# Kernel tuning notes

Measured on AMD Instinct MI355X. Metric: run time of the kernel, lower is better.

Reference implementation:

```python
import jax, jax.numpy as jnp
import numpy as np

MOMENTUM = 0.999
TEMP = 0.07
NUM_HARD_NEGS = 16
NUM_CLASSES = 20000


def _normalize(x, axis=-1, eps=1e-12):
    n = jnp.linalg.norm(x, axis=axis, keepdims=True)
    return x / jnp.maximum(n, eps)


def setup_inputs() -> dict:
    key = jax.random.key(0)
    k1, k2, k3, k4, k5 = jax.random.split(key, 5)
    B, K, Dp, De, C = 512, 8, 256, 512, NUM_CLASSES
    return {
        "part_features": jax.random.normal(k1, (B, K, Dp), dtype=jnp.float32),
        "embeddings": jax.random.normal(k2, (B, De), dtype=jnp.float32),
        "sat_emb": jax.random.normal(k3, (B, De), dtype=jnp.float32),
        "part_bank": jax.random.normal(k4, (C, K, Dp), dtype=jnp.float32) * 0.01,
        "embed_bank": jax.random.normal(k5, (C, De), dtype=jnp.float32) * 0.01,
        "labels": jnp.arange(B, dtype=jnp.int64),
    }


def reference(part_features, embeddings, sat_emb, part_bank, embed_bank, labels):
    m = MOMENTUM
    B = embeddings.shape[0]
    C = embed_bank.shape[0]

    # --- EMA scatter update (bank assumed initialized for all classes) ---
    # labels are distinct, so vectorized scatter == sequential python loop.
    new_part_bank = part_bank.at[labels].set(
        m * part_bank[labels] + (1.0 - m) * part_features)
    new_embed_bank = embed_bank.at[labels].set(
        m * embed_bank[labels] + (1.0 - m) * embeddings)

    # Banks are torch buffers updated under no_grad -> stop_gradient.
    eb = jax.lax.stop_gradient(new_embed_bank)

    # --- PrototypeNCE ---
    q = _normalize(embeddings)                      # [B, De]
    protos = _normalize(eb)                         # [C, De]
    sim = (q @ protos.T) / TEMP                     # [B, C]
    pos_sim = jnp.take_along_axis(sim, labels[:, None], axis=1)  # [B, 1]
    class_ids = jnp.arange(C)
    pos_mask = labels[:, None] == class_ids[None, :]
    neg_sim = jnp.where(pos_mask, -1e9, sim)
    hard_negs, _ = jax.lax.top_k(neg_sim, NUM_HARD_NEGS)          # [B, k]
    logits = jnp.concatenate([pos_sim, hard_negs], axis=1)       # [B, 1+k]
    nce_loss = jnp.mean(jax.nn.logsumexp(logits, axis=1) - logits[:, 0])

    # --- Cross-view prototype alignment ---
    p = _normalize(eb[labels])                      # [B, De]
    d = _normalize(embeddings)
    s = _normalize(sat_emb)
    align_loss = 0.5 * (jnp.mean(1.0 - jnp.sum(d * p, axis=-1))
                        + jnp.mean(1.0 - jnp.sum(s * p, axis=-1)))

    return new_part_bank, new_embed_bank, nce_loss, align_loss
```

## Files before the change

kernel.cpp:

```cpp
#include <hip/hip_runtime.h>
#include <math.h>

#define MOM 0.999f
#define ONE_M_MOM 0.001f
#define INV_TEMP (1.0f / 0.07f)
#define C_CLASSES 20000
#define B_SZ 512
#define DE 512
#define PART_ROW 2048
#define PART_BANK_N (C_CLASSES * PART_ROW)
#define EMB_BANK_N (C_CLASSES * DE)
#define NEG_INF (-3.0e38f)
#define NTILE 157
#define NT2 (NTILE * 2)
#define NGEMM (4 * NTILE)
#define NPART 2500

typedef __attribute__((ext_vector_type(8))) short short8;
typedef __attribute__((ext_vector_type(4))) float f32x4;

__device__ inline unsigned short f2bf_rne(float f) {
    unsigned u = __builtin_bit_cast(unsigned, f);
    return (unsigned short)((u + 0x7FFFu + ((u >> 16) & 1u)) >> 16);
}

__device__ inline float bf2f(unsigned short u) {
    return __builtin_bit_cast(float, (unsigned)u << 16);
}

__device__ inline void gload16(const void* g, void* l) {
    __builtin_amdgcn_global_load_lds(
        (const __attribute__((address_space(1))) unsigned int*)g,
        (__attribute__((address_space(3))) unsigned int*)l, 16, 0, 0);
}

__global__ void embed_qnorm(const float* __restrict__ ebank, const float* __restrict__ emb,
                            const int* __restrict__ labels, float* __restrict__ out_eb,
                            unsigned short* __restrict__ Bb, float* __restrict__ inv_norm,
                            float* __restrict__ q_hat, unsigned short* __restrict__ Ab,
                            int* __restrict__ counter) {
    int w = threadIdx.x >> 6, l = threadIdx.x & 63;
    int blk = blockIdx.x;
    if (blk == 0 && threadIdx.x == 0) *counter = 0;
    if (blk < 5000) {
        int c = blk * 4 + w;
        int m = -1;
#pragma unroll
        for (int k = 0; k < 8; ++k)
            if (labels[l + k * 64] == c) m = l + k * 64;
#pragma unroll
        for (int off = 32; off; off >>= 1) m = max(m, __shfl_xor(m, off));

        const float4* row = (const float4*)(ebank + ((long)c << 9));
        float4 v0 = row[2 * l], v1 = row[2 * l + 1];
        if (m >= 0) {
            const float4* nr = (const float4*)(emb + ((long)m << 9));
            float4 n0 = nr[2 * l], n1 = nr[2 * l + 1];
            v0.x = MOM * v0.x + ONE_M_MOM * n0.x;
            v0.y = MOM * v0.y + ONE_M_MOM * n0.y;
            v0.z = MOM * v0.z + ONE_M_MOM * n0.z;
            v0.w = MOM * v0.w + ONE_M_MOM * n0.w;
            v1.x = MOM * v1.x + ONE_M_MOM * n1.x;
            v1.y = MOM * v1.y + ONE_M_MOM * n1.y;
            v1.z = MOM * v1.z + ONE_M_MOM * n1.z;
            v1.w = MOM * v1.w + ONE_M_MOM * n1.w;
        }
        float4* orow = (float4*)(out_eb + ((long)c << 9));
        orow[2 * l] = v0; orow[2 * l + 1] = v1;
        float ss = v0.x * v0.x + v0.y * v0.y + v0.z * v0.z + v0.w * v0.w
                 + v1.x * v1.x + v1.y * v1.y + v1.z * v1.z + v1.w * v1.w;
#pragma unroll
        for (int off = 32; off; off >>= 1) ss += __shfl_xor(ss, off);
        if (l == 0) inv_norm[c] = 1.0f / fmaxf(sqrtf(ss), 1e-12f);
        short8 o;
        o[0] = (short)f2bf_rne(v0.x); o[1] = (short)f2bf_rne(v0.y);
        o[2] = (short)f2bf_rne(v0.z); o[3] = (short)f2bf_rne(v0.w);
        o[4] = (short)f2bf_rne(v1.x); o[5] = (short)f2bf_rne(v1.y);
        o[6] = (short)f2bf_rne(v1.z); o[7] = (short)f2bf_rne(v1.w);
        *(short8*)(Bb + ((long)c << 9) + l * 8) = o;
    } else {
        int b = (blk - 5000) * 4 + w;
        const float4* row = (const float4*)(emb + ((long)b << 9));
        float4 v0 = row[2 * l], v1 = row[2 * l + 1];
        float ss = v0.x * v0.x + v0.y * v0.y + v0.z * v0.z + v0.w * v0.w
                 + v1.x * v1.x + v1.y * v1.y + v1.z * v1.z + v1.w * v1.w;
#pragma unroll
        for (int off = 32; off; off >>= 1) ss += __shfl_xor(ss, off);
        float inv = 1.0f / fmaxf(sqrtf(ss), 1e-12f);
        v0.x *= inv; v0.y *= inv; v0.z *= inv; v0.w *= inv;
        v1.x *= inv; v1.y *= inv; v1.z *= inv; v1.w *= inv;
        float4* outq = (float4*)(q_hat + ((long)b << 9));
        outq[2 * l] = v0; outq[2 * l + 1] = v1;
        short8 o;
        o[0] = (short)f2bf_rne(v0.x); o[1] = (short)f2bf_rne(v0.y);
        o[2] = (short)f2bf_rne(v0.z); o[3] = (short)f2bf_rne(v0.w);
        o[4] = (short)f2bf_rne(v1.x); o[5] = (short)f2bf_rne(v1.y);
        o[6] = (short)f2bf_rne(v1.z); o[7] = (short)f2bf_rne(v1.w);
        *(short8*)(Ab + ((long)b << 9) + l * 8) = o;
    }
}

__global__ void __launch_bounds__(256)
part_gemm(const unsigned short* __restrict__ A, const unsigned short* __restrict__ B,
          const float* __restrict__ inv_norm, const int* __restrict__ labels,
          float* __restrict__ partials,
          const float4* __restrict__ pb, const float4* __restrict__ pf,
          float4* __restrict__ out_pb) {
    __shared__ unsigned short smem[128 * 130];

    if (blockIdx.x >= NGEMM) {
        int c0 = (blockIdx.x - NGEMM) * 8;
        int t = threadIdx.x;
        int* mbs = (int*)smem;
        if (t < 8) mbs[t] = -1;
        __syncthreads();
        int la = labels[t], lb = labels[t + 256];
#pragma unroll
        for (int r = 0; r < 8; ++r) {
            if (la == c0 + r) mbs[r] = t;
            if (lb == c0 + r) mbs[r] = t + 256;
        }
        __syncthreads();
        const float4* src = pb + (long)c0 * (PART_ROW / 4);
        float4* dst = out_pb + (long)c0 * (PART_ROW / 4);
        float4 v[16];
#pragma unroll
        for (int i = 0; i < 16; ++i) v[i] = src[t + i * 256];
#pragma unroll
        for (int i = 0; i < 16; ++i) {
            int mb = mbs[i >> 1];
            if (mb >= 0) {
                float4 n = pf[(long)mb * (PART_ROW / 4) + (t + (i & 1) * 256)];
                v[i].x = MOM * v[i].x + ONE_M_MOM * n.x;
                v[i].y = MOM * v[i].y + ONE_M_MOM * n.y;
                v[i].z = MOM * v[i].z + ONE_M_MOM * n.z;
                v[i].w = MOM * v[i].w + ONE_M_MOM * n.w;
            }
            dst[t + i * 256] = v[i];
        }
        return;
    }

    unsigned short* Asm = smem;
    unsigned short* Bsm = smem + 8192;

    const int t = threadIdx.x;
    const int w = t >> 6, l = t & 63;
    const int wr = w >> 1, wc = w & 1;

    int id = blockIdx.x;
    int xcd = id & 7, idx = id >> 3;
    int wg = (xcd < 4) ? xcd * 79 + idx : 316 + (xcd - 4) * 78 + idx;
    const int bm = wg & 3, bn = wg >> 2;

    f32x4 acc[4][4] = {};

    const int srow = t >> 3;
    const long swz = ((t & 7) ^ (srow & 7)) << 3;
    const unsigned short* Ag = A + ((long)(bm * 128 + srow) << 9) + swz;
    const unsigned short* Bg[4];
#pragma unroll
    for (int i = 0; i < 4; ++i) {
        int br = bn * 128 + i * 32 + srow;
        if (br > C_CLASSES - 1) br = C_CLASSES - 1;
        Bg[i] = B + ((long)br << 9) + swz;
    }
    char* Adst = (char*)Asm + (w << 10);
    char* Bdst = (char*)Bsm + (w << 10);

    const int fr = l & 15;
    const int s4 = l >> 4;
    const int swr0 = ((s4) ^ (fr & 7)) << 4;
    const int swr1 = ((4 + s4) ^ (fr & 7)) << 4;

    for (int kt = 0; kt < 8; ++kt) {
        const int ko = kt << 6;
#pragma unroll
        for (int i = 0; i < 4; ++i) {
            gload16(Ag + ko + ((long)i << 14), Adst + (i << 12));
            gload16(Bg[i] + ko, Bdst + (i << 12));
        }
        __syncthreads();
        short8 af[2][4], bf[2][4];
        const char* Abase = (const char*)Asm;
        const char* Bbase = (const char*)Bsm;
#pragma unroll
        for (int m = 0; m < 4; ++m) {
            int ra = (wr * 64 + m * 16 + fr) << 7;
            int rb = (wc * 64 + m * 16 + fr) << 7;
            af[0][m] = *(const short8*)(Abase + ra + swr0);
            af[1][m] = *(const short8*)(Abase + ra + swr1);
            bf[0][m] = *(const short8*)(Bbase + rb + swr0);
            bf[1][m] = *(const short8*)(Bbase + rb + swr1);
        }
#pragma unroll
        for (int kk = 0; kk < 2; ++kk)
#pragma unroll
            for (int m = 0; m < 4; ++m)
#pragma unroll
                for (int n = 0; n < 4; ++n)
                    acc[m][n] = __builtin_amdgcn_mfma_f32_16x16x32_bf16(
                        af[kk][m], bf[kk][n], acc[m][n], 0, 0, 0);
        __syncthreads();
    }

    unsigned short* stile = smem;
    const int r4 = s4 << 2;
#pragma unroll
    for (int n = 0; n < 4; ++n) {
        int ct = wc * 64 + fr + n * 16;
        int cg = bn * 128 + ct;
        bool ok = cg < C_CLASSES;
        float sc = ok ? inv_norm[cg] * INV_TEMP : 0.0f;
#pragma unroll
        for (int m = 0; m < 4; ++m) {
            int rt = wr * 64 + r4 + m * 16;
#pragma unroll
            for (int j = 0; j < 4; ++j) {
                float v = ok ? acc[m][n][j] * sc : NEG_INF;
                stile[(rt + j) * 130 + ct] = f2bf_rne(v);
            }
        }
    }
    __syncthreads();

    const int r = t >> 1, half = t & 1;
    const int gr = bm * 128 + r;
    const int lab = labels[gr];
    const int lab_l = lab - (bn << 7) - (half << 6);
    const unsigned short* bp = stile + r * 130 + half * 64;
    float tl[16];
#pragma unroll
    for (int j = 0; j < 16; ++j) tl[j] = NEG_INF;
    for (int c = 0; c < 64; ++c) {
        if (c == lab_l) continue;
        float v = bf2f(bp[c]);
        if (v > tl[15]) {
            tl[15] = v;
#pragma unroll
            for (int j = 15; j > 0; --j) {
                float a = tl[j - 1], bb = tl[j];
                if (bb > a) { tl[j - 1] = bb; tl[j] = a; }
            }
        }
    }
    float* op = partials + ((long)gr * NT2 + (bn << 1) + half) * 16;
#pragma unroll
    for (int j = 0; j < 16; ++j) op[j] = tl[j];
}

__global__ void __launch_bounds__(64)
merge_fin(const float* __restrict__ partials, const float* __restrict__ q_hat,
          const float* __restrict__ out_eb, const float* __restrict__ sat,
          const float* __restrict__ inv_norm, const int* __restrict__ labels,
          float* __restrict__ lnce, float* __restrict__ lalign,
          int* __restrict__ counter, float* __restrict__ out_losses) {
    int b = blockIdx.x;
    int l = threadIdx.x;
    const float4* pr4 = (const float4*)(partials + (long)b * (NT2 * 16));

    float tl[16];
#pragma unroll
    for (int j = 0; j < 16; ++j) tl[j] = NEG_INF;
    for (int i = l; i < NT2 * 4; i += 64) {
        float4 v4 = pr4[i];
        float vv[4] = {v4.x, v4.y, v4.z, v4.w};
#pragma unroll
        for (int q = 0; q < 4; ++q) {
            float v = vv[q];
            if (v > tl[15]) {
                tl[15] = v;
#pragma unroll
                for (int j = 15; j > 0; --j) {
                    float a = tl[j - 1], bb = tl[j];
                    if (bb > a) { tl[j - 1] = bb; tl[j] = a; }
                }
            }
        }
    }

    float M = 0.f, S = 0.f;
#pragma unroll 1
    for (int j = 0; j < 16; ++j) {
        float v = tl[0];
        float mx = v;
#pragma unroll
        for (int off = 32; off; off >>= 1) mx = fmaxf(mx, __shfl_xor(mx, off));
        unsigned long long ball = __ballot(v == mx);
        int win = (int)(__ffsll((unsigned long long)ball)) - 1;
        if (l == win) {
#pragma unroll
            for (int q = 0; q < 15; ++q) tl[q] = tl[q + 1];
            tl[15] = NEG_INF;
        }
        if (j == 0) { M = mx; S = 1.0f; }
        else S += expf(mx - M);
    }

    int lab = labels[b];
    const float4* qr = (const float4*)(q_hat + ((long)b << 9));
    const float4* er = (const float4*)(out_eb + ((long)lab << 9));
    const float4* sr = (const float4*)(sat + ((long)b << 9));
    float a1 = 0.f, a2 = 0.f, a3 = 0.f;
#pragma unroll
    for (int rr = 0; rr < 2; ++rr) {
        int j = 2 * l + rr;
        float4 d4 = qr[j], s4 = sr[j], e4 = er[j];
        a1 += d4.x * e4.x + d4.y * e4.y + d4.z * e4.z + d4.w * e4.w;
        a2 += s4.x * e4.x + s4.y * e4.y + s4.z * e4.z + s4.w * e4.w;
        a3 += s4.x * s4.x + s4.y * s4.y + s4.z * s4.z + s4.w * s4.w;
    }
#pragma unroll
    for (int off = 32; off; off >>= 1) {
        a1 += __shfl_xor(a1, off);
        a2 += __shfl_xor(a2, off);
        a3 += __shfl_xor(a3, off);
    }
    int done = 0;
    if (l == 0) {
        float invl = inv_norm[lab];
        float pos = a1 * invl * INV_TEMP;
        float mx2 = fmaxf(M, pos);
        float ssum = expf(M - mx2) * S + expf(pos - mx2);
        lnce[b] = logf(ssum) + mx2 - pos;
        float pd = a1 * invl;
        float ps = a2 * invl / fmaxf(sqrtf(a3), 1e-12f);
        lalign[b] = 1.0f - 0.5f * (pd + ps);
        __threadfence();
        done = (atomicAdd(counter, 1) == B_SZ - 1) ? 1 : 0;
    }
    done = __shfl(done, 0);
    if (done) {
        __threadfence();
        volatile const float* vn = lnce;
        volatile const float* va = lalign;
        float s1 = 0.f, s2 = 0.f;
#pragma unroll
        for (int k = 0; k < B_SZ / 64; ++k) {
            s1 += vn[l + k * 64];
            s2 += va[l + k * 64];
        }
#pragma unroll
        for (int off = 32; off; off >>= 1) {
            s1 += __shfl_xor(s1, off);
            s2 += __shfl_xor(s2, off);
        }
        if (l == 0) {
            out_losses[0] = s1 / (float)B_SZ;
            out_losses[1] = s2 / (float)B_SZ;
            *counter = 0;
        }
    }
}

extern "C" void kernel_launch(void* const* d_in, const int* in_sizes, int n_in,
                              void* d_out, int out_size, void* d_ws, size_t ws_size,
                              hipStream_t stream) {
    const float* pf = (const float*)d_in[0];
    const float* emb = (const float*)d_in[1];
    const float* sat = (const float*)d_in[2];
    const float* pb = (const float*)d_in[3];
    const float* ebank = (const float*)d_in[4];
    const int* labels = (const int*)d_in[5];

    float* out = (float*)d_out;
    float* out_pb = out;
    float* out_eb = out + PART_BANK_N;
    float* out_losses = out + PART_BANK_N + EMB_BANK_N;

    float* ws = (float*)d_ws;
    float* q_hat = ws;
    float* inv_norm = q_hat + (long)B_SZ * DE;
    int* counter = (int*)(inv_norm + C_CLASSES);
    float* lnce = (float*)(counter + 16);
    float* lalign = lnce + B_SZ;
    float* partials = lalign + B_SZ;
    unsigned short* Ab = (unsigned short*)(partials + (long)B_SZ * NT2 * 16);
    unsigned short* Bb = Ab + (long)B_SZ * DE;

    embed_qnorm<<<5000 + 128, 256, 0, stream>>>(ebank, emb, labels, out_eb, Bb, inv_norm,
                                                q_hat, Ab, counter);
    part_gemm<<<NGEMM + NPART, 256, 0, stream>>>(Ab, Bb, inv_norm, labels, partials,
                                                 (const float4*)pb, (const float4*)pf,
                                                 (float4*)out_pb);
    merge_fin<<<B_SZ, 64, 0, stream>>>(partials, q_hat, out_eb, sat, inv_norm,
                                       labels, lnce, lalign, counter, out_losses);
}
```

Before: 146.3 us.

## Persist part-bank copy blocks, merge half-tile top-k in GEMM, drop q_hat buffer

Result: slower. 157.1 us (+7.4%).

```diff
diff --git a/kernel.cpp b/kernel.cpp
--- a/kernel.cpp
+++ b/kernel.cpp
@@ -12,9 +12,9 @@
 #define EMB_BANK_N (C_CLASSES * DE)
 #define NEG_INF (-3.0e38f)
 #define NTILE 157
-#define NT2 (NTILE * 2)
 #define NGEMM (4 * NTILE)
-#define NPART 2500
+#define NCHUNK 2500
+#define NPARTB 512
 
 typedef __attribute__((ext_vector_type(8))) short short8;
 typedef __attribute__((ext_vector_type(4))) float f32x4;
@@ -37,8 +37,7 @@
 __global__ void embed_qnorm(const float* __restrict__ ebank, const float* __restrict__ emb,
                             const int* __restrict__ labels, float* __restrict__ out_eb,
                             unsigned short* __restrict__ Bb, float* __restrict__ inv_norm,
-                            float* __restrict__ q_hat, unsigned short* __restrict__ Ab,
-                            int* __restrict__ counter) {
+                            unsigned short* __restrict__ Ab, int* __restrict__ counter) {
     int w = threadIdx.x >> 6, l = threadIdx.x & 63;
     int blk = blockIdx.x;
     if (blk == 0 && threadIdx.x == 0) *counter = 0;
@@ -89,8 +88,6 @@
         float inv = 1.0f / fmaxf(sqrtf(ss), 1e-12f);
         v0.x *= inv; v0.y *= inv; v0.z *= inv; v0.w *= inv;
         v1.x *= inv; v1.y *= inv; v1.z *= inv; v1.w *= inv;
-        float4* outq = (float4*)(q_hat + ((long)b << 9));
-        outq[2 * l] = v0; outq[2 * l + 1] = v1;
         short8 o;
         o[0] = (short)f2bf_rne(v0.x); o[1] = (short)f2bf_rne(v0.y);
         o[2] = (short)f2bf_rne(v0.z); o[3] = (short)f2bf_rne(v0.w);
@@ -109,34 +106,37 @@
     __shared__ unsigned short smem[128 * 130];
 
     if (blockIdx.x >= NGEMM) {
-        int c0 = (blockIdx.x - NGEMM) * 8;
         int t = threadIdx.x;
         int* mbs = (int*)smem;
-        if (t < 8) mbs[t] = -1;
-        __syncthreads();
         int la = labels[t], lb = labels[t + 256];
-#pragma unroll
-        for (int r = 0; r < 8; ++r) {
-            if (la == c0 + r) mbs[r] = t;
-            if (lb == c0 + r) mbs[r] = t + 256;
-        }
-        __syncthreads();
-        const float4* src = pb + (long)c0 * (PART_ROW / 4);
-        float4* dst = out_pb + (long)c0 * (PART_ROW / 4);
-        float4 v[16];
-#pragma unroll
-        for (int i = 0; i < 16; ++i) v[i] = src[t + i * 256];
-#pragma unroll
-        for (int i = 0; i < 16; ++i) {
-            int mb = mbs[i >> 1];
-            if (mb >= 0) {
-                float4 n = pf[(long)mb * (PART_ROW / 4) + (t + (i & 1) * 256)];
-                v[i].x = MOM * v[i].x + ONE_M_MOM * n.x;
-                v[i].y = MOM * v[i].y + ONE_M_MOM * n.y;
-                v[i].z = MOM * v[i].z + ONE_M_MOM * n.z;
-                v[i].w = MOM * v[i].w + ONE_M_MOM * n.w;
+        for (int chunk = blockIdx.x - NGEMM; chunk < NCHUNK; chunk += NPARTB) {
+            int c0 = chunk * 8;
+            __syncthreads();
+            if (t < 8) mbs[t] = -1;
+            __syncthreads();
+#pragma unroll
+            for (int r = 0; r < 8; ++r) {
+                if (la == c0 + r) mbs[r] = t;
+                if (lb == c0 + r) mbs[r] = t + 256;
             }
-            dst[t + i * 256] = v[i];
+            __syncthreads();
+            const float4* src = pb + (long)c0 * (PART_ROW / 4);
+            float4* dst = out_pb + (long)c0 * (PART_ROW / 4);
+            float4 v[16];
+#pragma unroll
+            for (int i = 0; i < 16; ++i) v[i] = src[t + i * 256];
+#pragma unroll
+            for (int i = 0; i < 16; ++i) {
+                int mb = mbs[i >> 1];
+                if (mb >= 0) {
+                    float4 n = pf[(long)mb * (PART_ROW / 4) + (t + (i & 1) * 256)];
+                    v[i].x = MOM * v[i].x + ONE_M_MOM * n.x;
+                    v[i].y = MOM * v[i].y + ONE_M_MOM * n.y;
+                    v[i].z = MOM * v[i].z + ONE_M_MOM * n.z;
+                    v[i].w = MOM * v[i].w + ONE_M_MOM * n.w;
+                }
+                dst[t + i * 256] = v[i];
+            }
         }
         return;
     }
@@ -193,6 +193,7 @@
             bf[0][m] = *(const short8*)(Bbase + rb + swr0);
             bf[1][m] = *(const short8*)(Bbase + rb + swr1);
         }
+        __builtin_amdgcn_s_setprio(1);
 #pragma unroll
         for (int kk = 0; kk < 2; ++kk)
 #pragma unroll
@@ -201,6 +202,7 @@
                 for (int n = 0; n < 4; ++n)
                     acc[m][n] = __builtin_amdgcn_mfma_f32_16x16x32_bf16(
                         af[kk][m], bf[kk][n], acc[m][n], 0, 0, 0);
+        __builtin_amdgcn_s_setprio(0);
         __syncthreads();
     }
 
@@ -244,25 +246,38 @@
             }
         }
     }
-    float* op = partials + ((long)gr * NT2 + (bn << 1) + half) * 16;
-#pragma unroll
-    for (int j = 0; j < 16; ++j) op[j] = tl[j];
+    float ol[16];
+#pragma unroll
+    for (int j = 0; j < 16; ++j) ol[j] = __shfl_xor(tl[j], 1);
+    if (half == 0) {
+        float4 o0, o1, o2, o3;
+        o0.x = fmaxf(tl[0],  ol[15]); o0.y = fmaxf(tl[1],  ol[14]);
+        o0.z = fmaxf(tl[2],  ol[13]); o0.w = fmaxf(tl[3],  ol[12]);
+        o1.x = fmaxf(tl[4],  ol[11]); o1.y = fmaxf(tl[5],  ol[10]);
+        o1.z = fmaxf(tl[6],  ol[9]);  o1.w = fmaxf(tl[7],  ol[8]);
+        o2.x = fmaxf(tl[8],  ol[7]);  o2.y = fmaxf(tl[9],  ol[6]);
+        o2.z = fmaxf(tl[10], ol[5]);  o2.w = fmaxf(tl[11], ol[4]);
+        o3.x = fmaxf(tl[12], ol[3]);  o3.y = fmaxf(tl[13], ol[2]);
+        o3.z = fmaxf(tl[14], ol[1]);  o3.w = fmaxf(tl[15], ol[0]);
+        float4* op4 = (float4*)(partials + ((long)gr * NTILE + bn) * 16);
+        op4[0] = o0; op4[1] = o1; op4[2] = o2; op4[3] = o3;
+    }
 }
 
 __global__ void __launch_bounds__(64)
-merge_fin(const float* __restrict__ partials, const float* __restrict__ q_hat,
+merge_fin(const float* __restrict__ partials, const float* __restrict__ emb,
           const float* __restrict__ out_eb, const float* __restrict__ sat,
           const float* __restrict__ inv_norm, const int* __restrict__ labels,
           float* __restrict__ lnce, float* __restrict__ lalign,
           int* __restrict__ counter, float* __restrict__ out_losses) {
     int b = blockIdx.x;
     int l = threadIdx.x;
-    const float4* pr4 = (const float4*)(partials + (long)b * (NT2 * 16));
+    const float4* pr4 = (const float4*)(partials + (long)b * (NTILE * 16));
 
     float tl[16];
 #pragma unroll
     for (int j = 0; j < 16; ++j) tl[j] = NEG_INF;
-    for (int i = l; i < NT2 * 4; i += 64) {
+    for (int i = l; i < NTILE * 4; i += 64) {
         float4 v4 = pr4[i];
         float vv[4] = {v4.x, v4.y, v4.z, v4.w};
 #pragma unroll
@@ -298,10 +313,10 @@
     }
 
     int lab = labels[b];
-    const float4* qr = (const float4*)(q_hat + ((long)b << 9));
+    const float4* qr = (const float4*)(emb + ((long)b << 9));
     const float4* er = (const float4*)(out_eb + ((long)lab << 9));
     const float4* sr = (const float4*)(sat + ((long)b << 9));
-    float a1 = 0.f, a2 = 0.f, a3 = 0.f;
+    float a1 = 0.f, a2 = 0.f, a3 = 0.f, a4 = 0.f;
 #pragma unroll
     for (int rr = 0; rr < 2; ++rr) {
         int j = 2 * l + rr;
@@ -309,21 +324,24 @@
         a1 += d4.x * e4.x + d4.y * e4.y + d4.z * e4.z + d4.w * e4.w;
         a2 += s4.x * e4.x + s4.y * e4.y + s4.z * e4.z + s4.w * e4.w;
         a3 += s4.x * s4.x + s4.y * s4.y + s4.z * s4.z + s4.w * s4.w;
+        a4 += d4.x * d4.x + d4.y * d4.y + d4.z * d4.z + d4.w * d4.w;
     }
 #pragma unroll
     for (int off = 32; off; off >>= 1) {
         a1 += __shfl_xor(a1, off);
         a2 += __shfl_xor(a2, off);
         a3 += __shfl_xor(a3, off);
+        a4 += __shfl_xor(a4, off);
     }
     int done = 0;
     if (l == 0) {
         float invl = inv_norm[lab];
-        float pos = a1 * invl * INV_TEMP;
+        float invq = 1.0f / fmaxf(sqrtf(a4), 1e-12f);
+        float pos = a1 * invq * invl * INV_TEMP;
         float mx2 = fmaxf(M, pos);
         float ssum = expf(M - mx2) * S + expf(pos - mx2);
         lnce[b] = logf(ssum) + mx2 - pos;
-        float pd = a1 * invl;
+        float pd = a1 * invq * invl;
         float ps = a2 * invl / fmaxf(sqrtf(a3), 1e-12f);
         lalign[b] = 1.0f - 0.5f * (pd + ps);
         __threadfence();
@@ -369,20 +387,19 @@
     float* out_losses = out + PART_BANK_N + EMB_BANK_N;
 
     float* ws = (float*)d_ws;
-    float* q_hat = ws;
-    float* inv_norm = q_hat + (long)B_SZ * DE;
+    float* inv_norm = ws;
     int* counter = (int*)(inv_norm + C_CLASSES);
     float* lnce = (float*)(counter + 16);
     float* lalign = lnce + B_SZ;
     float* partials = lalign + B_SZ;
-    unsigned short* Ab = (unsigned short*)(partials + (long)B_SZ * NT2 * 16);
+    unsigned short* Ab = (unsigned short*)(partials + (long)B_SZ * NTILE * 16);
     unsigned short* Bb = Ab + (long)B_SZ * DE;
 
     embed_qnorm<<<5000 + 128, 256, 0, stream>>>(ebank, emb, labels, out_eb, Bb, inv_norm,
-                                                q_hat, Ab, counter);
-    part_gemm<<<NGEMM + NPART, 256, 0, stream>>>(Ab, Bb, inv_norm, labels, partials,
-                                                 (const float4*)pb, (const float4*)pf,
-                                                 (float4*)out_pb);
-    merge_fin<<<B_SZ, 64, 0, stream>>>(partials, q_hat, out_eb, sat, inv_norm,
+                                                Ab, counter);
+    part_gemm<<<NGEMM + NPARTB, 256, 0, stream>>>(Ab, Bb, inv_norm, labels, partials,
+                                                  (const float4*)pb, (const float4*)pf,
+                                                  (float4*)out_pb);
+    merge_fin<<<B_SZ, 64, 0, stream>>>(partials, emb, out_eb, sat, inv_norm,
                                        labels, lnce, lalign, counter, out_losses);
 }
```
